# Optimization experiments

Hardware: AMD Instinct MI355X
Metric: run time of the kernel (lower is better)

## Reference

```python
import jax, jax.numpy as jnp
import numpy as np
from jax import lax

OBS_DIM = 128      # proj_size == obs_dim
HIDDEN = 1024      # cell size
OUT_SAMPLES = 8192 # last 64 timesteps * 128
B, T = 64, 2048


def _lstmp_layer(x, Wih, Whh, bih, bhh, Whr):
    """One LSTM layer with projection (PyTorch proj_size semantics).
    x: [B, T, in]; Wih: [4H, in]; Whh: [4H, P]; Whr: [P, H].
    Gate order i, f, g, o. Returns [B, T, P]."""
    Bv = x.shape[0]
    H = Whh.shape[0] // 4
    P = Whr.shape[0]
    # input contribution for all timesteps in one GEMM: [B, T, 4H]
    xg = jnp.einsum('bti,gi->btg', x, Wih) + bih

    def step(carry, xg_t):
        h, c = carry                       # h: [B,P], c: [B,H]
        g = xg_t + h @ Whh.T + bhh         # [B, 4H]
        i, f, gg, o = jnp.split(g, 4, axis=-1)
        c = jax.nn.sigmoid(f) * c + jax.nn.sigmoid(i) * jnp.tanh(gg)
        h = (jax.nn.sigmoid(o) * jnp.tanh(c)) @ Whr.T  # project to [B,P]
        return (h, c), h

    h0 = jnp.zeros((Bv, P), x.dtype)
    c0 = jnp.zeros((Bv, H), x.dtype)
    (_, _), hs = lax.scan(step, (h0, c0), jnp.swapaxes(xg, 0, 1))
    return jnp.swapaxes(hs, 0, 1)          # [B, T, P]


def setup_inputs() -> dict:
    key = jax.random.key(0)
    ks = jax.random.split(key, 12)
    s = 1.0 / np.sqrt(HIDDEN)
    P, H = OBS_DIM, HIDDEN
    d = {
        'x': jax.random.normal(ks[0], (B, T, OBS_DIM), dtype=jnp.float32),
        # layer 0: input size = obs_dim
        'Wih0': jax.random.uniform(ks[1], (4 * H, OBS_DIM), minval=-s, maxval=s),
        'Whh0': jax.random.uniform(ks[2], (4 * H, P), minval=-s, maxval=s),
        'bih0': jax.random.uniform(ks[3], (4 * H,), minval=-s, maxval=s),
        'bhh0': jax.random.uniform(ks[4], (4 * H,), minval=-s, maxval=s),
        'Whr0': jax.random.uniform(ks[5], (P, H), minval=-s, maxval=s),
        # layer 1: input size = proj_size = obs_dim
        'Wih1': jax.random.uniform(ks[6], (4 * H, P), minval=-s, maxval=s),
        'Whh1': jax.random.uniform(ks[7], (4 * H, P), minval=-s, maxval=s),
        'bih1': jax.random.uniform(ks[8], (4 * H,), minval=-s, maxval=s),
        'bhh1': jax.random.uniform(ks[9], (4 * H,), minval=-s, maxval=s),
        'Whr1': jax.random.uniform(ks[10], (P, H), minval=-s, maxval=s),
    }
    return d


def reference(x, Wih0, Whh0, bih0, bhh0, Whr0, Wih1, Whh1, bih1, bhh1, Whr1):
    xb = x.reshape(x.shape[0], -1, OBS_DIM)
    h1 = _lstmp_layer(xb, Wih0, Whh0, bih0, bhh0, Whr0)
    h2 = _lstmp_layer(h1, Wih1, Whh1, bih1, bhh1, Whr1)
    outs = h2.reshape(h2.shape[0], -1)
    return outs[:, -OUT_SAMPLES:]
```

## Files before the change

kernel.cpp:

```cpp
#include <hip/hip_runtime.h>
#include <hip/hip_fp16.h>


typedef _Float16 f16;
typedef _Float16 f16x4 __attribute__((ext_vector_type(4)));
typedef _Float16 f16x8 __attribute__((ext_vector_type(8)));
typedef float f32x4 __attribute__((ext_vector_type(4)));
typedef unsigned long long u64;
struct U128 { u64 lo, hi; };

#define TSTEPS 2048
#define NW 32
#define TIMEOUT_TICKS 200000000ull

#define BSW_OFF  0ull
#define BSW_SZ   (64ull*32768ull*2ull)
#define WHR_OFF  (BSW_OFF + BSW_SZ)
#define WHR_SZ   (64ull*4096ull*2ull)
#define BIAS_OFF (WHR_OFF + WHR_SZ)
#define BIAS_SZ  (8192ull*4ull)
#define HACC_OFF (BIAS_OFF + BIAS_SZ)
#define HACC_SZ  (2ull*8ull*8192ull*4ull)
#define FLAG_OFF (HACC_OFF + HACC_SZ)
#define FLAG_SZ  (512ull)
#define WS_NEED  (FLAG_OFF + FLAG_SZ)

__device__ __forceinline__ float sigm(float v) {
  float e = __builtin_amdgcn_exp2f(-1.4426950408889634f * v);
  return __builtin_amdgcn_rcpf(1.0f + e);
}
__device__ __forceinline__ float tanh_(float v) {
  float a = fabsf(v);
  float e = __builtin_amdgcn_exp2f(-2.8853900817779268f * a);
  float r = (1.0f - e) * __builtin_amdgcn_rcpf(1.0f + e);
  return copysignf(r, v);
}

__device__ __forceinline__ u64 ald64(const void* p) {
  return __hip_atomic_load((const u64*)p, __ATOMIC_RELAXED, __HIP_MEMORY_SCOPE_AGENT);
}
__device__ __forceinline__ unsigned ald32u(const unsigned* p) {
  return __hip_atomic_load(p, __ATOMIC_RELAXED, __HIP_MEMORY_SCOPE_AGENT);
}
__device__ __forceinline__ void ast32f(float* p, float v) {
  __hip_atomic_store((unsigned*)p, __builtin_bit_cast(unsigned, v),
                     __ATOMIC_RELAXED, __HIP_MEMORY_SCOPE_AGENT);
}
__device__ __forceinline__ void ast32u(unsigned* p, unsigned v) {
  __hip_atomic_store(p, v, __ATOMIC_RELAXED, __HIP_MEMORY_SCOPE_AGENT);
}
__device__ __forceinline__ f32x4 ald_f32x4(const float* p) {
  U128 u; u.lo = ald64(p); u.hi = ald64(p + 2);
  return __builtin_bit_cast(f32x4, u);
}
__device__ __forceinline__ void aadd_f32(float* p, float v) {
  (void)__hip_atomic_fetch_add(p, v, __ATOMIC_RELAXED, __HIP_MEMORY_SCOPE_AGENT);
}
__device__ __forceinline__ void vm_drain() {
  asm volatile("s_waitcnt vmcnt(0)" ::: "memory");
}

__global__ void lstm_setup(
    const float* __restrict__ Wih0, const float* __restrict__ Whh0,
    const float* __restrict__ bih0, const float* __restrict__ bhh0,
    const float* __restrict__ Whr0,
    const float* __restrict__ Wih1, const float* __restrict__ Whh1,
    const float* __restrict__ bih1, const float* __restrict__ bhh1,
    const float* __restrict__ Whr1,
    f16* __restrict__ Bsw, f16* __restrict__ Whrsw, float* __restrict__ bias,
    float* __restrict__ hacc, unsigned* __restrict__ flags)
{
  const int blk = blockIdx.x, tid = threadIdx.x;
  if (blk < 64) {
    const int lyr = blk >> 5, w = blk & 31;
    const float* Whh = lyr ? Whh1 : Whh0;
    const float* Wih = lyr ? Wih1 : Wih0;
    f16* dst = Bsw + (size_t)blk * 32768;
    for (int e = tid; e < 32768; e += 256) {
      int i = e & 7, l = (e >> 3) & 63, ntG = (e >> 9) & 7, ks = e >> 12;
      int k  = ks * 32 + (l >> 4) * 8 + i;
      int rl = ntG * 16 + (l & 15);
      int grow = (rl >> 5) * 1024 + w * 32 + (rl & 31);
      float v = (k < 128) ? Whh[grow * 128 + k] : Wih[grow * 128 + (k - 128)];
      dst[e] = (f16)v;
    }
  } else if (blk < 128) {
    const int q = blk - 64, lyr = q >> 5, w = q & 31;
    const float* Whr = lyr ? Whr1 : Whr0;
    f16* dst = Whrsw + (size_t)q * 4096;
    for (int e = tid; e < 4096; e += 256) {
      int i = e & 7, l = (e >> 3) & 63, pnG = e >> 9;
      int p = pnG * 16 + (l & 15);
      int hg = w * 32 + (l >> 4) * 8 + i;
      dst[e] = (f16)Whr[p * 1024 + hg];
    }
  } else if (blk == 128) {
    for (int e = tid; e < 8192; e += 256) {
      int lyr = e >> 12, j = e & 4095;
      bias[e] = lyr ? (bih1[j] + bhh1[j]) : (bih0[j] + bhh0[j]);
    }
  } else {
    for (int e = tid; e < 2 * 8 * 8192; e += 256) ast32f(hacc + e, 0.f);
    if (tid < 128) ast32u(flags + tid, 0u);
  }
}

__global__ __launch_bounds__(256, 1) void lstm_main(
    const float* __restrict__ x, float* __restrict__ out,
    const f16* __restrict__ Bsw, const f16* __restrict__ Whrsw,
    const float* __restrict__ bias, float* __restrict__ hacc,
    unsigned* __restrict__ flags)
{
  const int tid = threadIdx.x;
  const int lane = tid & 63, wv = tid >> 6;
  const int wy = wv >> 1, wx = wv & 1;
  const int l15 = lane & 15, lg = lane >> 4;
  const int w = blockIdx.x & 31, lyr = blockIdx.x >> 5;

  const u64 tstart = __builtin_amdgcn_s_memrealtime();
  bool tmo = false;

  __shared__ __align__(16) f16 h_lds[64][136];
  __shared__ __align__(16) f16 x1_lds[64][136];
  __shared__ __align__(16) f16 s_lds[64][40];

  f16x8 bf[8][4];
  {
    const f16* bsl = Bsw + (size_t)(lyr * NW + w) * 32768;
#pragma unroll
    for (int ks = 0; ks < 8; ++ks)
#pragma unroll
      for (int ntl = 0; ntl < 4; ++ntl)
        bf[ks][ntl] = *(const f16x8*)(bsl + (((ks * 8 + (ntl * 2 + wx)) * 64 + lane) * 8));
  }
  f16x8 wf[4];
  {
    const f16* wsl = Whrsw + (size_t)(lyr * NW + w) * 4096;
#pragma unroll
    for (int pnl = 0; pnl < 4; ++pnl)
      wf[pnl] = *(const f16x8*)(wsl + (((pnl * 2 + wx) * 64 + lane) * 8));
  }
  float bias_r[4];
#pragma unroll
  for (int ntl = 0; ntl < 4; ++ntl)
    bias_r[ntl] = bias[lyr * 4096 + ntl * 1024 + w * 32 + wx * 16 + l15];

  float c[2][4] = {{0.f,0.f,0.f,0.f},{0.f,0.f,0.f,0.f}};

  unsigned* f0 = flags;
  unsigned* f1 = flags + 32;
  unsigned* myf = lyr ? f1 : f0;
  float* myacc = hacc + (size_t)lyr * 8 * 8192;
  float* h1a   = hacc;
  __syncthreads();

  for (int t = 0; t <= TSTEPS; ++t) {
    if (lyr == 0 && t == TSTEPS) break;
    const bool tail = (t == TSTEPS);

    f32x4 acc[2][4];
#pragma unroll
    for (int mtl = 0; mtl < 2; ++mtl)
#pragma unroll
      for (int ntl = 0; ntl < 4; ++ntl) {
        f32x4 b4 = {bias_r[ntl], bias_r[ntl], bias_r[ntl], bias_r[ntl]};
        acc[mtl][ntl] = b4;
      }
    if (lyr == 0) {
#pragma unroll
      for (int mtl = 0; mtl < 2; ++mtl) {
        const float* xp = x + ((size_t)((wy * 2 + mtl) * 16 + l15) * TSTEPS + t) * 128 + lg * 8;
#pragma unroll
        for (int ks2 = 0; ks2 < 4; ++ks2) {
          f32x4 v0 = *(const f32x4*)(xp + ks2 * 32);
          f32x4 v1 = *(const f32x4*)(xp + ks2 * 32 + 4);
          f16x8 hx;
          hx[0]=(f16)v0[0]; hx[1]=(f16)v0[1]; hx[2]=(f16)v0[2]; hx[3]=(f16)v0[3];
          hx[4]=(f16)v1[0]; hx[5]=(f16)v1[1]; hx[6]=(f16)v1[2]; hx[7]=(f16)v1[3];
#pragma unroll
          for (int ntl = 0; ntl < 4; ++ntl)
            acc[mtl][ntl] = __builtin_amdgcn_mfma_f32_16x16x32_f16(hx, bf[4 + ks2][ntl], acc[mtl][ntl], 0, 0, 0);
        }
      }
    }

    {
      int itc = 0;
      for (;;) {
        bool ok = true;
        if (lane < 32) {
          ok = ald32u(myf + lane) >= (unsigned)t;
        } else {
          const int l2 = lane - 32;
          if (lyr == 0) ok = (t < 4) || (ald32u(f1 + l2) >= (unsigned)(t - 3));
          else          ok = tail || (ald32u(f0 + l2) >= (unsigned)(t + 1));
        }
        if (__all(ok)) break;
        if ((++itc & 63) == 0) {
          if ((__builtin_amdgcn_s_memrealtime() - tstart) > TIMEOUT_TICKS) { tmo = true; break; }
        }
      }
    }
    asm volatile("" ::: "memory");

    {
      const int b = tid >> 2, pb = (tid & 3) * 32;
      const float* hp = myacc + (size_t)((t + 7) & 7) * 8192 + b * 128 + pb;
      f32x4 hv4[8];
#pragma unroll
      for (int k = 0; k < 8; ++k) hv4[k] = ald_f32x4(hp + k * 4);
      f32x4 x1v[8];
      if (lyr == 1 && !tail) {
        const float* xp1 = h1a + (size_t)(t & 7) * 8192 + b * 128 + pb;
#pragma unroll
        for (int k = 0; k < 8; ++k) x1v[k] = ald_f32x4(xp1 + k * 4);
      }
      if (lyr == 1 && t >= TSTEPS - 63 && (tid & 3) == (w >> 3))
        *(f32x4*)(out + (size_t)b * 8192 + (t - 1 - (TSTEPS - 64)) * 128 + w * 4) = hv4[w & 7];
#pragma unroll
      for (int k = 0; k < 8; ++k) {
        f16x4 h16;
#pragma unroll
        for (int e = 0; e < 4; ++e) h16[e] = (f16)hv4[k][e];
        *(f16x4*)(&h_lds[b][pb + k * 4]) = h16;
      }
      if (lyr == 1 && !tail) {
#pragma unroll
        for (int k = 0; k < 8; ++k) {
          f16x4 h16;
#pragma unroll
          for (int e = 0; e < 4; ++e) h16[e] = (f16)x1v[k][e];
          *(f16x4*)(&x1_lds[b][pb + k * 4]) = h16;
        }
      }
      if (!tail)
        ast32f(myacc + (size_t)((t + 4) & 7) * 8192 + b * 128 + w * 4 + (tid & 3), 0.f);
    }
    if (tail) break;
    __syncthreads();

#pragma unroll
    for (int mtl = 0; mtl < 2; ++mtl) {
#pragma unroll
      for (int ks = 0; ks < 4; ++ks) {
        f16x8 af = *(const f16x8*)(&h_lds[(wy * 2 + mtl) * 16 + l15][ks * 32 + lg * 8]);
#pragma unroll
        for (int ntl = 0; ntl < 4; ++ntl)
          acc[mtl][ntl] = __builtin_amdgcn_mfma_f32_16x16x32_f16(af, bf[ks][ntl], acc[mtl][ntl], 0, 0, 0);
      }
      if (lyr == 1) {
#pragma unroll
        for (int ks2 = 0; ks2 < 4; ++ks2) {
          f16x8 xf = *(const f16x8*)(&x1_lds[(wy * 2 + mtl) * 16 + l15][ks2 * 32 + lg * 8]);
#pragma unroll
          for (int ntl = 0; ntl < 4; ++ntl)
            acc[mtl][ntl] = __builtin_amdgcn_mfma_f32_16x16x32_f16(xf, bf[4 + ks2][ntl], acc[mtl][ntl], 0, 0, 0);
        }
      }
#pragma unroll
      for (int r = 0; r < 4; ++r) {
        float gi = acc[mtl][0][r], gf = acc[mtl][1][r];
        float gg = acc[mtl][2][r], go = acc[mtl][3][r];
        float cc = sigm(gf) * c[mtl][r] + sigm(gi) * tanh_(gg);
        c[mtl][r] = cc;
        float s = sigm(go) * tanh_(cc);
        s_lds[(wy * 2 + mtl) * 16 + lg * 4 + r][wx * 16 + l15] = (f16)s;
      }
    }
    __syncthreads();

    {
      float* dst = myacc + (size_t)(t & 7) * 8192;
#pragma unroll
      for (int pml = 0; pml < 2; ++pml) {
        f16x8 ap = *(const f16x8*)(&s_lds[(wy * 2 + pml) * 16 + l15][lg * 8]);
#pragma unroll
        for (int pnl = 0; pnl < 4; ++pnl) {
          f32x4 z = {0.f, 0.f, 0.f, 0.f};
          f32x4 pa = __builtin_amdgcn_mfma_f32_16x16x32_f16(ap, wf[pnl], z, 0, 0, 0);
          const int p = (pnl * 2 + wx) * 16 + l15;
#pragma unroll
          for (int r = 0; r < 4; ++r) {
            const int b = (wy * 2 + pml) * 16 + lg * 4 + r;
            aadd_f32(dst + b * 128 + p, pa[r]);
          }
        }
      }
    }
    vm_drain();
    __syncthreads();
    if (tid == 0) ast32u(myf + w, (unsigned)(t + 1));
  }

  if (tmo && tid == 0) out[0] = 12345.0f;
}

extern "C" void kernel_launch(void* const* d_in, const int* in_sizes, int n_in,
                              void* d_out, int out_size, void* d_ws, size_t ws_size,
                              hipStream_t stream)
{
  const float* x    = (const float*)d_in[0];
  const float* Wih0 = (const float*)d_in[1];
  const float* Whh0 = (const float*)d_in[2];
  const float* bih0 = (const float*)d_in[3];
  const float* bhh0 = (const float*)d_in[4];
  const float* Whr0 = (const float*)d_in[5];
  const float* Wih1 = (const float*)d_in[6];
  const float* Whh1 = (const float*)d_in[7];
  const float* bih1 = (const float*)d_in[8];
  const float* bhh1 = (const float*)d_in[9];
  const float* Whr1 = (const float*)d_in[10];

  if (ws_size < WS_NEED) return;

  char* ws = (char*)d_ws;
  f16*      Bsw   = (f16*)(ws + BSW_OFF);
  f16*      Whrsw = (f16*)(ws + WHR_OFF);
  float*    bias  = (float*)(ws + BIAS_OFF);
  float*    hacc  = (float*)(ws + HACC_OFF);
  unsigned* flags = (unsigned*)(ws + FLAG_OFF);

  lstm_setup<<<130, 256, 0, stream>>>(Wih0, Whh0, bih0, bhh0, Whr0,
                                      Wih1, Whh1, bih1, bhh1, Whr1,
                                      Bsw, Whrsw, bias, hacc, flags);
  lstm_main<<<64, 256, 0, stream>>>(x, (float*)d_out, Bsw, Whrsw, bias,
                                    hacc, flags);
}
```

Measured before the change: 17.04 ms.

## Load recurrent h directly into MFMA fragments, drop LDS staging and a barrier

Each wave now reads the previous h and layer-1 input straight from the global accumulation ring into MFMA A-fragments, instead of staging them through shared memory. This removes two LDS arrays and one __syncthreads per step, at the cost of redundant global reads across waves. The ring-slot zeroing moves after the flag publish, output writes for the last timesteps are reorganised with a separate tail copy, and a dummy FMA loop is added to the spin-wait to throttle polling.

```diff
diff --git a/kernel.cpp b/kernel.cpp
--- a/kernel.cpp
+++ b/kernel.cpp
@@ -120,8 +120,6 @@
   const u64 tstart = __builtin_amdgcn_s_memrealtime();
   bool tmo = false;
 
-  __shared__ __align__(16) f16 h_lds[64][136];
-  __shared__ __align__(16) f16 x1_lds[64][136];
   __shared__ __align__(16) f16 s_lds[64][40];
 
   f16x8 bf[8][4];
@@ -186,6 +184,7 @@
 
     {
       int itc = 0;
+      float b0 = (float)lane, b1 = b0 + 1.f, b2 = b0 + 2.f, b3 = b0 + 3.f;
       for (;;) {
         bool ok = true;
         if (lane < 32) {
@@ -195,6 +194,14 @@
           if (lyr == 0) ok = (t < 4) || (ald32u(f1 + l2) >= (unsigned)(t - 3));
           else          ok = tail || (ald32u(f0 + l2) >= (unsigned)(t + 1));
         }
+#pragma unroll
+        for (int q = 0; q < 32; ++q) {
+          b0 = __builtin_fmaf(b0, 1.000001f, 0.5f);
+          b1 = __builtin_fmaf(b1, 1.000001f, 0.5f);
+          b2 = __builtin_fmaf(b2, 1.000001f, 0.5f);
+          b3 = __builtin_fmaf(b3, 1.000001f, 0.5f);
+        }
+        asm volatile("" : "+v"(b0), "+v"(b1), "+v"(b2), "+v"(b3));
         if (__all(ok)) break;
         if ((++itc & 63) == 0) {
           if ((__builtin_amdgcn_s_memrealtime() - tstart) > TIMEOUT_TICKS) { tmo = true; break; }
@@ -203,59 +210,66 @@
     }
     asm volatile("" ::: "memory");
 
-    {
-      const int b = tid >> 2, pb = (tid & 3) * 32;
-      const float* hp = myacc + (size_t)((t + 7) & 7) * 8192 + b * 128 + pb;
-      f32x4 hv4[8];
-#pragma unroll
-      for (int k = 0; k < 8; ++k) hv4[k] = ald_f32x4(hp + k * 4);
-      f32x4 x1v[8];
-      if (lyr == 1 && !tail) {
-        const float* xp1 = h1a + (size_t)(t & 7) * 8192 + b * 128 + pb;
-#pragma unroll
-        for (int k = 0; k < 8; ++k) x1v[k] = ald_f32x4(xp1 + k * 4);
-      }
-      if (lyr == 1 && t >= TSTEPS - 63 && (tid & 3) == (w >> 3))
-        *(f32x4*)(out + (size_t)b * 8192 + (t - 1 - (TSTEPS - 64)) * 128 + w * 4) = hv4[w & 7];
-#pragma unroll
-      for (int k = 0; k < 8; ++k) {
-        f16x4 h16;
-#pragma unroll
-        for (int e = 0; e < 4; ++e) h16[e] = (f16)hv4[k][e];
-        *(f16x4*)(&h_lds[b][pb + k * 4]) = h16;
-      }
-      if (lyr == 1 && !tail) {
-#pragma unroll
-        for (int k = 0; k < 8; ++k) {
-          f16x4 h16;
-#pragma unroll
-          for (int e = 0; e < 4; ++e) h16[e] = (f16)x1v[k][e];
-          *(f16x4*)(&x1_lds[b][pb + k * 4]) = h16;
-        }
-      }
-      if (!tail)
-        ast32f(myacc + (size_t)((t + 4) & 7) * 8192 + b * 128 + w * 4 + (tid & 3), 0.f);
-    }
-    if (tail) break;
-    __syncthreads();
+    const float* hp  = myacc + (size_t)((t + 7) & 7) * 8192;
+    const float* x1p = h1a + (size_t)(t & 7) * 8192;
+
+    if (tail) {
+      if (w == 0 && wx == 0) {
+#pragma unroll
+        for (int mtl = 0; mtl < 2; ++mtl) {
+          const int bm = (wy * 2 + mtl) * 16 + l15;
+#pragma unroll
+          for (int ks = 0; ks < 4; ++ks) {
+            f32x4 lo = ald_f32x4(hp + bm * 128 + ks * 32 + lg * 8);
+            f32x4 hi = ald_f32x4(hp + bm * 128 + ks * 32 + lg * 8 + 4);
+            float* op = out + (size_t)bm * 8192 + 63 * 128 + ks * 32 + lg * 8;
+            *(f32x4*)op = lo;
+            *(f32x4*)(op + 4) = hi;
+          }
+        }
+      }
+      break;
+    }
 
 #pragma unroll
     for (int mtl = 0; mtl < 2; ++mtl) {
+      const int bm = (wy * 2 + mtl) * 16 + l15;
+      f16x8 hf[4];
 #pragma unroll
       for (int ks = 0; ks < 4; ++ks) {
-        f16x8 af = *(const f16x8*)(&h_lds[(wy * 2 + mtl) * 16 + l15][ks * 32 + lg * 8]);
+        f32x4 lo = ald_f32x4(hp + bm * 128 + ks * 32 + lg * 8);
+        f32x4 hi = ald_f32x4(hp + bm * 128 + ks * 32 + lg * 8 + 4);
+        if (lyr == 1 && w == 0 && wx == 0 && t >= TSTEPS - 63) {
+          float* op = out + (size_t)bm * 8192 + (size_t)(t - 1 - (TSTEPS - 64)) * 128 + ks * 32 + lg * 8;
+          *(f32x4*)op = lo;
+          *(f32x4*)(op + 4) = hi;
+        }
+        f16x8 hv;
+        hv[0]=(f16)lo[0]; hv[1]=(f16)lo[1]; hv[2]=(f16)lo[2]; hv[3]=(f16)lo[3];
+        hv[4]=(f16)hi[0]; hv[5]=(f16)hi[1]; hv[6]=(f16)hi[2]; hv[7]=(f16)hi[3];
+        hf[ks] = hv;
+      }
+#pragma unroll
+      for (int ks = 0; ks < 4; ++ks)
 #pragma unroll
         for (int ntl = 0; ntl < 4; ++ntl)
-          acc[mtl][ntl] = __builtin_amdgcn_mfma_f32_16x16x32_f16(af, bf[ks][ntl], acc[mtl][ntl], 0, 0, 0);
-      }
+          acc[mtl][ntl] = __builtin_amdgcn_mfma_f32_16x16x32_f16(hf[ks], bf[ks][ntl], acc[mtl][ntl], 0, 0, 0);
       if (lyr == 1) {
+        f16x8 xf[4];
 #pragma unroll
         for (int ks2 = 0; ks2 < 4; ++ks2) {
-          f16x8 xf = *(const f16x8*)(&x1_lds[(wy * 2 + mtl) * 16 + l15][ks2 * 32 + lg * 8]);
+          f32x4 lo = ald_f32x4(x1p + bm * 128 + ks2 * 32 + lg * 8);
+          f32x4 hi = ald_f32x4(x1p + bm * 128 + ks2 * 32 + lg * 8 + 4);
+          f16x8 hv;
+          hv[0]=(f16)lo[0]; hv[1]=(f16)lo[1]; hv[2]=(f16)lo[2]; hv[3]=(f16)lo[3];
+          hv[4]=(f16)hi[0]; hv[5]=(f16)hi[1]; hv[6]=(f16)hi[2]; hv[7]=(f16)hi[3];
+          xf[ks2] = hv;
+        }
+#pragma unroll
+        for (int ks2 = 0; ks2 < 4; ++ks2)
 #pragma unroll
           for (int ntl = 0; ntl < 4; ++ntl)
-            acc[mtl][ntl] = __builtin_amdgcn_mfma_f32_16x16x32_f16(xf, bf[4 + ks2][ntl], acc[mtl][ntl], 0, 0, 0);
-        }
+            acc[mtl][ntl] = __builtin_amdgcn_mfma_f32_16x16x32_f16(xf[ks2], bf[4 + ks2][ntl], acc[mtl][ntl], 0, 0, 0);
       }
 #pragma unroll
       for (int r = 0; r < 4; ++r) {
@@ -290,6 +304,11 @@
     vm_drain();
     __syncthreads();
     if (tid == 0) ast32u(myf + w, (unsigned)(t + 1));
+
+    {
+      const int b = tid >> 2;
+      ast32f(myacc + (size_t)((t + 4) & 7) * 8192 + b * 128 + w * 4 + (tid & 3), 0.f);
+    }
   }
 
   if (tmo && tid == 0) out[0] = 12345.0f;
```

Measured after the change: 23.60 ms. 1.39x slower.
